# Optimization experiments

Measured on AMD Instinct MI355X. Metric: run time of the kernel, lower is better.

## Reference

```python
import jax, jax.numpy as jnp
import numpy as np

N_NODES = 8192
N_EDGES = 262144
N_REL = 8
NUM_CLASSES = 151
EMB = 256
BOX = 1024
HID = 512
OUT = 256
N_TASKS = 2


def setup_inputs() -> dict:
    key = jax.random.key(0)
    ks = jax.random.split(key, 20)
    w = lambda k, shape: jax.random.normal(k, shape, dtype=jnp.float32) * 0.02
    return {
        "box_features": jax.random.normal(ks[0], (N_NODES, BOX), dtype=jnp.float32),
        "pred_labels": jax.random.randint(ks[1], (N_NODES,), 0, NUM_CLASSES),
        "edge_index": jax.random.randint(ks[2], (2, N_EDGES), 0, N_NODES),
        "edge_type": jax.random.randint(ks[3], (N_EDGES,), 0, N_REL),
        "nodes_per_graph": 128,
        "emb_table": w(ks[4], (NUM_CLASSES, EMB)),
        "W_lin": w(ks[5], (BOX + EMB, HID)),
        "b_lin": jnp.zeros((HID,), jnp.float32),
        "rel_W1": w(ks[6], (N_REL, HID, HID)),
        "root_W1": w(ks[7], (HID, HID)),
        "b1": jnp.zeros((HID,), jnp.float32),
        "rel_W2": w(ks[8], (N_REL, HID, OUT)),
        "root_W2": w(ks[9], (HID, OUT)),
        "b2": jnp.zeros((OUT,), jnp.float32),
        "Wc1": w(ks[10], (OUT, OUT)),
        "bc1": jnp.zeros((OUT,), jnp.float32),
        "Wc2": w(ks[11], (OUT, N_TASKS)),
        "bc2": jnp.zeros((N_TASKS,), jnp.float32),
    }


def rgcn_conv(x, src, dst, etype, rel_W, root_W, b):
    """PyG RGCNConv: per-relation mean aggregation + root weight + bias."""
    R, _, out_dim = rel_W.shape
    N = x.shape[0]
    transformed = jnp.einsum('ni,rio->rno', x, rel_W)      # [R, N, out]
    msg = transformed[etype, src]                           # [E, out] gather per edge
    seg = etype * N + dst                                   # (relation, dst) segment id
    sums = jax.ops.segment_sum(msg, seg, num_segments=R * N)
    cnt = jax.ops.segment_sum(jnp.ones((msg.shape[0],), x.dtype), seg, num_segments=R * N)
    mean = sums / jnp.maximum(cnt, 1.0)[:, None]
    agg = mean.reshape(R, N, out_dim).sum(0)                # sum over relations
    return agg + x @ root_W + b


def reference(box_features, pred_labels, edge_index, edge_type, nodes_per_graph,
              emb_table, W_lin, b_lin, rel_W1, root_W1, b1, rel_W2, root_W2, b2,
              Wc1, bc1, Wc2, bc2):
    src, dst = edge_index[0], edge_index[1]
    # obj embedding + concat with box features
    x = jnp.concatenate([box_features, emb_table[pred_labels]], axis=-1)  # [N, 1280]
    x = x @ W_lin + b_lin                                                  # [N, 512]
    x = jax.nn.relu(rgcn_conv(x, src, dst, edge_type, rel_W1, root_W1, b1))
    x = rgcn_conv(x, src, dst, edge_type, rel_W2, root_W2, b2)             # [N, 256]
    # mean graph pooling over equal-size graphs
    B = x.shape[0] // nodes_per_graph
    pooled = x.reshape(B, nodes_per_graph, -1).mean(axis=1)                # [B, 256]
    # classifier (dropout is identity in eval)
    y_logits = (pooled @ Wc1 + bc1) @ Wc2 + bc2                            # [B, n_tasks]
    y_prob = jax.nn.softmax(y_logits, axis=-1)
    return y_logits, y_prob
```

## Files before the change

### kernel.cpp

```cpp
#include <hip/hip_runtime.h>
#include <cstdint>

#define NNODES 8192
#define NEDGES 262144
#define NRELS  8
#define EMBD   256
#define BOXD   1024
#define HIDD   512
#define OUTD   256
#define NSEG   (NRELS * NNODES)
#define K0DIM  (BOXD + EMBD)
#define KSDIM  (NRELS * HIDD + HIDD)

#define PREP_X0_END   8192
#define PREP_TR_END   (8192 + 2944)
#define PREP_WB_END   (8192 + 2944 + 18)
#define PREP_TOTAL    (8192 + 2944 + 18 + 1024)

using bf16x8 = __attribute__((ext_vector_type(8))) short;
using f32x4  = __attribute__((ext_vector_type(4))) float;
using us4    = __attribute__((ext_vector_type(4))) unsigned short;

__device__ __forceinline__ unsigned short f2b(float f) {
    union { float f; uint32_t u; } v; v.f = f;
    uint32_t r = v.u + 0x7FFFu + ((v.u >> 16) & 1u);
    return (unsigned short)(r >> 16);
}

__device__ __forceinline__ us4 cvt4(f32x4 v) {
    us4 u;
    u[0] = f2b(v[0]); u[1] = f2b(v[1]); u[2] = f2b(v[2]); u[3] = f2b(v[3]);
    return u;
}

__device__ __forceinline__ float b2f_lo(uint32_t w) {
    union { uint32_t u; float f; } v; v.u = w << 16; return v.f;
}
__device__ __forceinline__ float b2f_hi(uint32_t w) {
    union { uint32_t u; float f; } v; v.u = w & 0xffff0000u; return v.f;
}

__global__ __launch_bounds__(256) void k_prep(
        const float* __restrict__ box, const int* __restrict__ labels,
        const float* __restrict__ emb,
        const float* __restrict__ W_lin, const float* __restrict__ rel_W1,
        const float* __restrict__ root_W1, const float* __restrict__ rel_W2,
        const float* __restrict__ root_W2,
        const float* __restrict__ Wc1, const float* __restrict__ bc1,
        const float* __restrict__ Wc2, const float* __restrict__ bc2,
        const float* __restrict__ b2,
        const int* __restrict__ etype, const int* __restrict__ edst,
        unsigned short* __restrict__ X0, unsigned short* __restrict__ W0t,
        unsigned short* __restrict__ W1t, float* __restrict__ Wbig,
        float* __restrict__ bbig, int* __restrict__ cnt) {
    int bid = blockIdx.x;
    if (bid < PREP_X0_END) {
        int n = bid;
        int lab = labels[n];
        const f32x4* b = (const f32x4*)(box + (size_t)n * BOXD);
        const f32x4* e = (const f32x4*)(emb + (size_t)lab * EMBD);
        us4* o = (us4*)(X0 + (size_t)n * K0DIM);
        for (int j = threadIdx.x; j < K0DIM / 4; j += 256) {
            f32x4 v = (j < BOXD / 4) ? b[j] : e[j - BOXD / 4];
            o[j] = cvt4(v);
        }
    } else if (bid < PREP_TR_END) {
        __shared__ float t[32][33];
        int lb = bid - PREP_X0_END;
        const float* src; unsigned short* dst; int No, ld, kOff, kb, ob;
        if (lb < 640)       { int g = lb;        src = W_lin;   dst = W0t; No = 512; ld = K0DIM; kOff = 0;    kb = g % 40;  ob = g / 40; }
        else if (lb < 2688) { int g = lb - 640;  src = rel_W1;  dst = W1t; No = 512; ld = KSDIM; kOff = 0;    kb = g % 128; ob = g / 128; }
        else                { int g = lb - 2688; src = root_W1; dst = W1t; No = 512; ld = KSDIM; kOff = 4096; kb = g % 16;  ob = g / 16; }
        int kt = kb * 32, ot = ob * 32;
        int tx = threadIdx.x & 31, ty = threadIdx.x >> 5;
#pragma unroll
        for (int i = 0; i < 4; i++) {
            int k = kt + ty + i * 8;
            t[ty + i * 8][tx] = src[(size_t)k * No + ot + tx];
        }
        __syncthreads();
#pragma unroll
        for (int i = 0; i < 4; i++) {
            int o = ot + ty + i * 8;
            dst[(size_t)o * ld + kOff + kt + tx] = f2b(t[tx][ty + i * 8]);
        }
    } else if (bid < PREP_WB_END) {
        __shared__ float ws0[256], ws1[256];
        __shared__ float r0[256], r1[256];
        int g = bid - PREP_TR_END;
        int i = threadIdx.x;
        float w0 = 0.f, w1 = 0.f;
        for (int o = 0; o < 256; o++) {
            float c = Wc1[i * 256 + o];
            w0 += c * Wc2[o * 2 + 0];
            w1 += c * Wc2[o * 2 + 1];
        }
        ws0[i] = w0; ws1[i] = w1;
        __syncthreads();
        int k = g * 256 + i;
        const float* row = (k < 4096) ? rel_W2 + (size_t)k * 256
                                      : root_W2 + (size_t)(k - 4096) * 256;
        float s0 = 0.f, s1 = 0.f;
        for (int o = 0; o < 256; o++) {
            float v = row[o];
            s0 += v * ws0[o];
            s1 += v * ws1[o];
        }
        Wbig[k * 2 + 0] = s0;
        Wbig[k * 2 + 1] = s1;
        if (g == 0) {
            r0[i] = b2[i] * ws0[i] + bc1[i] * Wc2[i * 2 + 0];
            r1[i] = b2[i] * ws1[i] + bc1[i] * Wc2[i * 2 + 1];
            __syncthreads();
            for (int s = 128; s > 0; s >>= 1) {
                if (i < s) { r0[i] += r0[i + s]; r1[i] += r1[i + s]; }
                __syncthreads();
            }
            if (i == 0) { bbig[0] = r0[0] + bc2[0]; bbig[1] = r1[0] + bc2[1]; }
        }
    } else {
        int e = (bid - PREP_WB_END) * 256 + threadIdx.x;
        atomicAdd(&cnt[etype[e] * NNODES + edst[e]], 1);
    }
}

__global__ __launch_bounds__(1024) void k_scan(const int* __restrict__ cnt,
                                               int* __restrict__ segstart) {
    __shared__ int part[1024];
    __shared__ int sup[16];
    __shared__ int supx[16];
    int t = threadIdx.x;
    int base = t * 64;
    int s = 0;
    for (int i = 0; i < 64; i++) s += cnt[base + i];
    part[t] = s;
    __syncthreads();
    if (t < 16) {
        int a = 0;
        for (int i = 0; i < 64; i++) a += part[t * 64 + i];
        sup[t] = a;
    }
    __syncthreads();
    if (t == 0) {
        int a = 0;
        for (int i = 0; i < 16; i++) { supx[i] = a; a += sup[i]; }
    }
    __syncthreads();
    int a = supx[t >> 6];
    for (int i = (t & ~63); i < t; i++) a += part[i];
    for (int i = 0; i < 64; i++) { segstart[base + i] = a; a += cnt[base + i]; }
    if (t == 1023) segstart[NSEG] = a;
}

__global__ void k_scatter(const int* __restrict__ etype, const int* __restrict__ esrc,
                          const int* __restrict__ edst, const int* __restrict__ segstart,
                          int* __restrict__ cursor, int* __restrict__ esorted) {
    int e = blockIdx.x * 256 + threadIdx.x;
    if (e >= NEDGES) return;
    int key = etype[e] * NNODES + edst[e];
    int pos = atomicAdd(&cursor[key], 1);
    esorted[segstart[key] + pos] = esrc[e];
}

__global__ __launch_bounds__(256) void k_aggregate(
        const unsigned short* __restrict__ x, const int* __restrict__ segstart,
        const int* __restrict__ esorted, unsigned short* __restrict__ Xin) {
    int seg = blockIdx.x * 4 + (threadIdx.x >> 6);
    int lane = threadIdx.x & 63;
    int r = seg >> 13;
    int dstn = seg & (NNODES - 1);
    float a[8] = {0, 0, 0, 0, 0, 0, 0, 0};
    float b[8] = {0, 0, 0, 0, 0, 0, 0, 0};
    int s0 = segstart[seg], s1 = segstart[seg + 1];
    int t = s0;
    for (; t + 2 <= s1; t += 2) {
        uint4 v0 = *(const uint4*)(x + (size_t)esorted[t] * HIDD + lane * 8);
        uint4 v1 = *(const uint4*)(x + (size_t)esorted[t + 1] * HIDD + lane * 8);
        a[0] += b2f_lo(v0.x); a[1] += b2f_hi(v0.x);
        a[2] += b2f_lo(v0.y); a[3] += b2f_hi(v0.y);
        a[4] += b2f_lo(v0.z); a[5] += b2f_hi(v0.z);
        a[6] += b2f_lo(v0.w); a[7] += b2f_hi(v0.w);
        b[0] += b2f_lo(v1.x); b[1] += b2f_hi(v1.x);
        b[2] += b2f_lo(v1.y); b[3] += b2f_hi(v1.y);
        b[4] += b2f_lo(v1.z); b[5] += b2f_hi(v1.z);
        b[6] += b2f_lo(v1.w); b[7] += b2f_hi(v1.w);
    }
    if (t < s1) {
        uint4 v0 = *(const uint4*)(x + (size_t)esorted[t] * HIDD + lane * 8);
        a[0] += b2f_lo(v0.x); a[1] += b2f_hi(v0.x);
        a[2] += b2f_lo(v0.y); a[3] += b2f_hi(v0.y);
        a[4] += b2f_lo(v0.z); a[5] += b2f_hi(v0.z);
        a[6] += b2f_lo(v0.w); a[7] += b2f_hi(v0.w);
    }
    float iv = (s1 > s0) ? (1.0f / (float)(s1 - s0)) : 1.0f;
#pragma unroll
    for (int j = 0; j < 8; j++) a[j] = (a[j] + b[j]) * iv;
    uint4 u;
    u.x = (uint32_t)f2b(a[0]) | ((uint32_t)f2b(a[1]) << 16);
    u.y = (uint32_t)f2b(a[2]) | ((uint32_t)f2b(a[3]) << 16);
    u.z = (uint32_t)f2b(a[4]) | ((uint32_t)f2b(a[5]) << 16);
    u.w = (uint32_t)f2b(a[6]) | ((uint32_t)f2b(a[7]) << 16);
    *(uint4*)(Xin + (size_t)dstn * KSDIM + r * HIDD + lane * 8) = u;
}

__global__ __launch_bounds__(256) void k_aggpool(
        const unsigned short* __restrict__ x, const int* __restrict__ segstart,
        const int* __restrict__ esorted, float* __restrict__ PXp) {
    __shared__ float red[4][512];
    int b = blockIdx.x;
    int wave = threadIdx.x >> 6, lane = threadIdx.x & 63;
    if (b < 2048) {
        int q = b & 3, r = (b >> 2) & 7, g = b >> 5;
        float a[8] = {0, 0, 0, 0, 0, 0, 0, 0};
        int segbase = r * NNODES + g * 128 + q * 32 + wave * 8;
#pragma unroll 1
        for (int i = 0; i < 8; ++i) {
            int s0 = segstart[segbase + i], s1 = segstart[segbase + i + 1];
            if (s0 == s1) continue;
            float p[8] = {0, 0, 0, 0, 0, 0, 0, 0};
            for (int t = s0; t < s1; ++t) {
                uint4 v = *(const uint4*)(x + (size_t)esorted[t] * HIDD + lane * 8);
                p[0] += b2f_lo(v.x); p[1] += b2f_hi(v.x);
                p[2] += b2f_lo(v.y); p[3] += b2f_hi(v.y);
                p[4] += b2f_lo(v.z); p[5] += b2f_hi(v.z);
                p[6] += b2f_lo(v.w); p[7] += b2f_hi(v.w);
            }
            float w = 1.0f / (128.0f * (float)(s1 - s0));
#pragma unroll
            for (int j = 0; j < 8; j++) a[j] += p[j] * w;
        }
#pragma unroll
        for (int j = 0; j < 8; j++) red[wave][lane * 8 + j] = a[j];
        __syncthreads();
        for (int c = threadIdx.x; c < 512; c += 256) {
            float s = red[0][c] + red[1][c] + red[2][c] + red[3][c];
            PXp[((size_t)q * 64 + g) * KSDIM + r * 512 + c] = s;
        }
    } else {
        int t2 = b - 2048;
        int g = t2 >> 2, q = t2 & 3;
        float a[8] = {0, 0, 0, 0, 0, 0, 0, 0};
        int n0 = g * 128 + q * 32 + wave * 8;
#pragma unroll
        for (int i = 0; i < 8; ++i) {
            uint4 v = *(const uint4*)(x + (size_t)(n0 + i) * HIDD + lane * 8);
            a[0] += b2f_lo(v.x); a[1] += b2f_hi(v.x);
            a[2] += b2f_lo(v.y); a[3] += b2f_hi(v.y);
            a[4] += b2f_lo(v.z); a[5] += b2f_hi(v.z);
            a[6] += b2f_lo(v.w); a[7] += b2f_hi(v.w);
        }
#pragma unroll
        for (int j = 0; j < 8; j++) red[wave][lane * 8 + j] = a[j];
        __syncthreads();
        for (int c = threadIdx.x; c < 512; c += 256) {
            float s = red[0][c] + red[1][c] + red[2][c] + red[3][c];
            PXp[((size_t)q * 64 + g) * KSDIM + 4096 + c] = s * (1.0f / 128.0f);
        }
    }
}

__global__ __launch_bounds__(512, 4) void k_gemm(
        const unsigned short* __restrict__ A,
        const unsigned short* __restrict__ Bt,
        float* __restrict__ P,
        int M, int N, int K, int Kc) {
    __shared__ unsigned short As[2][128 * 64];
    __shared__ unsigned short Bs[2][128 * 64];
    const int tid = threadIdx.x;
    const int lane = tid & 63, wid = tid >> 6;
    const int tiles_m = M >> 7;
    const int tm = blockIdx.x % tiles_m, tn = blockIdx.x / tiles_m;
    const int m0 = tm << 7, n0 = tn << 7;
    const int wr = wid >> 2, wc = wid & 3;
    const int k0 = blockIdx.y * Kc;

    f32x4 acc[4][2];
#pragma unroll
    for (int i = 0; i < 4; i++)
#pragma unroll
        for (int j = 0; j < 2; j++) acc[i][j] = (f32x4){0.f, 0.f, 0.f, 0.f};

    const int rowg = tid >> 3;
    const int srcc = (tid & 7) ^ (rowg & 7);
    const unsigned short* gA = A  + (size_t)(m0 + rowg) * K + k0 + srcc * 8;
    const unsigned short* gB = Bt + (size_t)(n0 + rowg) * K + k0 + srcc * 8;
    const int ldsbase = wid * 512;

    auto stage = [&](int bsel, int kt) {
#pragma unroll
        for (int i = 0; i < 2; ++i) {
            __builtin_amdgcn_global_load_lds(
                (const __attribute__((address_space(1))) void*)(gA + kt + i * 64 * K),
                (__attribute__((address_space(3))) void*)&As[bsel][i * 4096 + ldsbase], 16, 0, 0);
            __builtin_amdgcn_global_load_lds(
                (const __attribute__((address_space(1))) void*)(gB + kt + i * 64 * K),
                (__attribute__((address_space(3))) void*)&Bs[bsel][i * 4096 + ldsbase], 16, 0, 0);
        }
    };

    const int arow = wr * 64 + (lane & 15);
    const int brow = wc * 32 + (lane & 15);
    const int l7 = lane & 7;
    const int c0 = lane >> 4;

    const int nt = Kc >> 6;
    int cur = 0;
    stage(0, 0);
    asm volatile("s_waitcnt vmcnt(0)" ::: "memory");
    __builtin_amdgcn_s_barrier();

    for (int t = 0; t < nt; ++t) {
        if (t + 1 < nt) stage(cur ^ 1, (t + 1) * 64);
#pragma unroll
        for (int s4 = 0; s4 < 2; ++s4) {
            const int slot = (c0 + s4 * 4) ^ l7;
            bf16x8 af[4], bfr[2];
#pragma unroll
            for (int m = 0; m < 4; m++)
                af[m] = *(const bf16x8*)&As[cur][(arow + m * 16) * 64 + slot * 8];
#pragma unroll
            for (int n = 0; n < 2; n++)
                bfr[n] = *(const bf16x8*)&Bs[cur][(brow + n * 16) * 64 + slot * 8];
#pragma unroll
            for (int m = 0; m < 4; m++)
#pragma unroll
                for (int n = 0; n < 2; n++)
                    acc[m][n] = __builtin_amdgcn_mfma_f32_16x16x32_bf16(af[m], bfr[n], acc[m][n], 0, 0, 0);
        }
        if (t + 1 < nt) {
            asm volatile("s_waitcnt vmcnt(0)" ::: "memory");
            __builtin_amdgcn_s_barrier();
            cur ^= 1;
        }
    }

    float* Pout = P + (size_t)blockIdx.y * M * N;
    const int crow0 = m0 + wr * 64 + (lane >> 4) * 4;
    const int ccol0 = n0 + wc * 32 + (lane & 15);
#pragma unroll
    for (int n = 0; n < 2; n++) {
        int col = ccol0 + n * 16;
#pragma unroll
        for (int m = 0; m < 4; m++)
#pragma unroll
            for (int r = 0; r < 4; r++)
                Pout[(size_t)(crow0 + m * 16 + r) * N + col] = acc[m][n][r];
    }
}

template <int RELU, int WROOT>
__global__ void k_reduce_bf(const float* __restrict__ P, const float* __restrict__ bias,
                            unsigned short* __restrict__ xbf, unsigned short* __restrict__ Xin,
                            int MN) {
    int idx = (blockIdx.x * 256 + threadIdx.x) * 4;
    f32x4 v = *(const f32x4*)&P[idx];
    v += *(const f32x4*)&P[(size_t)MN + idx];
    v += *(const f32x4*)&bias[idx & 511];
    if (RELU) {
#pragma unroll
        for (int j = 0; j < 4; j++) v[j] = fmaxf(v[j], 0.f);
    }
    us4 u = cvt4(v);
    *(us4*)&xbf[idx] = u;
    if (WROOT) {
        int row = idx >> 9, col = idx & 511;
        *(us4*)&Xin[(size_t)row * KSDIM + NRELS * HIDD + col] = u;
    }
}

__global__ void k_logits(const float* __restrict__ PXp, const float* __restrict__ Wbig,
                         const float* __restrict__ bbig, float* __restrict__ out) {
    __shared__ float r0[256], r1[256];
    int g = blockIdx.x, tid = threadIdx.x;
    const float* p0 = PXp + ((size_t)0 * 64 + g) * KSDIM;
    const float* p1 = PXp + ((size_t)1 * 64 + g) * KSDIM;
    const float* p2 = PXp + ((size_t)2 * 64 + g) * KSDIM;
    const float* p3 = PXp + ((size_t)3 * 64 + g) * KSDIM;
    float s0 = 0.f, s1 = 0.f;
#pragma unroll
    for (int i = 0; i < 18; i++) {
        int k = i * 256 + tid;
        float px = p0[k] + p1[k] + p2[k] + p3[k];
        s0 += px * Wbig[k * 2 + 0];
        s1 += px * Wbig[k * 2 + 1];
    }
    r0[tid] = s0; r1[tid] = s1;
    __syncthreads();
    for (int s = 128; s > 0; s >>= 1) {
        if (tid < s) { r0[tid] += r0[tid + s]; r1[tid] += r1[tid + s]; }
        __syncthreads();
    }
    if (tid == 0) {
        float l0 = r0[0] + bbig[0], l1 = r1[0] + bbig[1];
        out[g * 2 + 0] = l0;
        out[g * 2 + 1] = l1;
        float m = fmaxf(l0, l1);
        float e0 = expf(l0 - m), e1 = expf(l1 - m);
        float inv = 1.0f / (e0 + e1);
        out[128 + g * 2 + 0] = e0 * inv;
        out[128 + g * 2 + 1] = e1 * inv;
    }
}

extern "C" void kernel_launch(void* const* d_in, const int* in_sizes, int n_in,
                              void* d_out, int out_size, void* d_ws, size_t ws_size,
                              hipStream_t stream) {
    const float* box     = (const float*)d_in[0];
    const int*   labels  = (const int*)d_in[1];
    const int*   eidx    = (const int*)d_in[2];
    const int*   etype   = (const int*)d_in[3];
    const float* emb     = (const float*)d_in[5];
    const float* W_lin   = (const float*)d_in[6];
    const float* b_lin   = (const float*)d_in[7];
    const float* rel_W1  = (const float*)d_in[8];
    const float* root_W1 = (const float*)d_in[9];
    const float* b1      = (const float*)d_in[10];
    const float* rel_W2  = (const float*)d_in[11];
    const float* root_W2 = (const float*)d_in[12];
    const float* b2      = (const float*)d_in[13];
    const float* Wc1     = (const float*)d_in[14];
    const float* bc1     = (const float*)d_in[15];
    const float* Wc2     = (const float*)d_in[16];
    const float* bc2     = (const float*)d_in[17];
    const int* esrc = eidx;
    const int* edst = eidx + NEDGES;

    char* ws = (char*)d_ws;
    size_t off = 0;
    auto alloc = [&](size_t bytes) -> char* {
        char* p = ws + off;
        off += (bytes + 255) & ~(size_t)255;
        return p;
    };
    float* Pp = (float*)alloc((size_t)2 * NNODES * HIDD * 4);
    unsigned short* Xin = (unsigned short*)alloc((size_t)NNODES * KSDIM * 2);
    unsigned short* X0  = Xin;
    unsigned short* xbf = (unsigned short*)alloc((size_t)NNODES * HIDD * 2);
    unsigned short* W0t = (unsigned short*)alloc((size_t)HIDD * K0DIM * 2);
    unsigned short* W1t = (unsigned short*)alloc((size_t)HIDD * KSDIM * 2);
    float* PXp    = (float*)alloc((size_t)4 * 64 * KSDIM * 4);
    float* Wbig   = (float*)alloc((size_t)KSDIM * 2 * 4);
    float* bbig   = (float*)alloc(2 * 4);
    int*   cnt     = (int*)alloc((size_t)NSEG * 4);
    int*   cursor  = (int*)alloc((size_t)NSEG * 4);
    int*   segst   = (int*)alloc((size_t)(NSEG + 1) * 4);
    int*   esorted = (int*)alloc((size_t)NEDGES * 4);
    if (off > ws_size) return;

    float* out = (float*)d_out;
    const int MN = NNODES * HIDD;

    hipMemsetAsync(cnt, 0, (size_t)2 * NSEG * 4, stream);
    k_prep<<<PREP_TOTAL, 256, 0, stream>>>(
        box, labels, emb, W_lin, rel_W1, root_W1, rel_W2, root_W2,
        Wc1, bc1, Wc2, bc2, b2, etype, edst,
        X0, W0t, W1t, Wbig, bbig, cnt);
    k_scan<<<1, 1024, 0, stream>>>(cnt, segst);
    k_scatter<<<NEDGES / 256, 256, 0, stream>>>(etype, esrc, edst, segst, cursor, esorted);

    k_gemm<<<dim3((NNODES / 128) * (HIDD / 128), 2), 512, 0, stream>>>(
        X0, W0t, Pp, NNODES, HIDD, K0DIM, K0DIM / 2);
    k_reduce_bf<0, 1><<<MN / 1024, 256, 0, stream>>>(Pp, b_lin, xbf, Xin, MN);

    k_aggregate<<<NSEG / 4, 256, 0, stream>>>(xbf, segst, esorted, Xin);
    k_gemm<<<dim3((NNODES / 128) * (HIDD / 128), 2), 512, 0, stream>>>(
        Xin, W1t, Pp, NNODES, HIDD, KSDIM, KSDIM / 2);
    k_reduce_bf<1, 0><<<MN / 1024, 256, 0, stream>>>(Pp, b1, xbf, Xin, MN);

    k_aggpool<<<2048 + 256, 256, 0, stream>>>(xbf, segst, esorted, PXp);
    k_logits<<<64, 256, 0, stream>>>(PXp, Wbig, bbig, out);
}
```

Before: 258.7 us.

## Replace second-layer gather-pool with dense coefficient-matrix GEMM

The final aggregate-and-pool step is recast as a dense matrix product. A per-(relation, graph) by source-node coefficient matrix is built during the edge scatter with atomics, converted to bf16, and multiplied by a transposed hidden-feature matrix using the existing split-K GEMM. The root term is folded into the logits kernel. This removes the irregular per-edge gathers in pooling, but adds a 16MB memset, atomic scatter traffic, a conversion pass, a transpose, and bf16 rounding of the coefficients.

```diff
diff --git a/kernel.cpp b/kernel.cpp
--- a/kernel.cpp
+++ b/kernel.cpp
@@ -16,6 +16,8 @@
 #define PREP_TR_END   (8192 + 2944)
 #define PREP_WB_END   (8192 + 2944 + 18)
 #define PREP_TOTAL    (8192 + 2944 + 18 + 1024)
+
+#define PX_SPLITS 16
 
 using bf16x8 = __attribute__((ext_vector_type(8))) short;
 using f32x4  = __attribute__((ext_vector_type(4))) float;
@@ -154,12 +156,23 @@
 
 __global__ void k_scatter(const int* __restrict__ etype, const int* __restrict__ esrc,
                           const int* __restrict__ edst, const int* __restrict__ segstart,
-                          int* __restrict__ cursor, int* __restrict__ esorted) {
+                          int* __restrict__ cursor, int* __restrict__ esorted,
+                          float* __restrict__ Cf) {
     int e = blockIdx.x * 256 + threadIdx.x;
     if (e >= NEDGES) return;
-    int key = etype[e] * NNODES + edst[e];
+    int r = etype[e], d = edst[e], s = esrc[e];
+    int key = r * NNODES + d;
     int pos = atomicAdd(&cursor[key], 1);
-    esorted[segstart[key] + pos] = esrc[e];
+    esorted[segstart[key] + pos] = s;
+    int cntv = segstart[key + 1] - segstart[key];
+    float w = 1.0f / (128.0f * (float)cntv);
+    atomicAdd(&Cf[(size_t)(r * 64 + (d >> 7)) * NNODES + s], w);
+}
+
+__global__ void k_c2bf(const float* __restrict__ Cf, unsigned short* __restrict__ Cbf) {
+    int idx = (blockIdx.x * 256 + threadIdx.x) * 4;
+    f32x4 v = *(const f32x4*)&Cf[idx];
+    *(us4*)&Cbf[idx] = cvt4(v);
 }
 
 __global__ __launch_bounds__(256) void k_aggregate(
@@ -203,60 +216,18 @@
     *(uint4*)(Xin + (size_t)dstn * KSDIM + r * HIDD + lane * 8) = u;
 }
 
-__global__ __launch_bounds__(256) void k_aggpool(
-        const unsigned short* __restrict__ x, const int* __restrict__ segstart,
-        const int* __restrict__ esorted, float* __restrict__ PXp) {
-    __shared__ float red[4][512];
+__global__ void k_xT(const unsigned short* __restrict__ xbf, unsigned short* __restrict__ xT) {
+    __shared__ unsigned short t[32][33];
     int b = blockIdx.x;
-    int wave = threadIdx.x >> 6, lane = threadIdx.x & 63;
-    if (b < 2048) {
-        int q = b & 3, r = (b >> 2) & 7, g = b >> 5;
-        float a[8] = {0, 0, 0, 0, 0, 0, 0, 0};
-        int segbase = r * NNODES + g * 128 + q * 32 + wave * 8;
-#pragma unroll 1
-        for (int i = 0; i < 8; ++i) {
-            int s0 = segstart[segbase + i], s1 = segstart[segbase + i + 1];
-            if (s0 == s1) continue;
-            float p[8] = {0, 0, 0, 0, 0, 0, 0, 0};
-            for (int t = s0; t < s1; ++t) {
-                uint4 v = *(const uint4*)(x + (size_t)esorted[t] * HIDD + lane * 8);
-                p[0] += b2f_lo(v.x); p[1] += b2f_hi(v.x);
-                p[2] += b2f_lo(v.y); p[3] += b2f_hi(v.y);
-                p[4] += b2f_lo(v.z); p[5] += b2f_hi(v.z);
-                p[6] += b2f_lo(v.w); p[7] += b2f_hi(v.w);
-            }
-            float w = 1.0f / (128.0f * (float)(s1 - s0));
-#pragma unroll
-            for (int j = 0; j < 8; j++) a[j] += p[j] * w;
-        }
-#pragma unroll
-        for (int j = 0; j < 8; j++) red[wave][lane * 8 + j] = a[j];
-        __syncthreads();
-        for (int c = threadIdx.x; c < 512; c += 256) {
-            float s = red[0][c] + red[1][c] + red[2][c] + red[3][c];
-            PXp[((size_t)q * 64 + g) * KSDIM + r * 512 + c] = s;
-        }
-    } else {
-        int t2 = b - 2048;
-        int g = t2 >> 2, q = t2 & 3;
-        float a[8] = {0, 0, 0, 0, 0, 0, 0, 0};
-        int n0 = g * 128 + q * 32 + wave * 8;
-#pragma unroll
-        for (int i = 0; i < 8; ++i) {
-            uint4 v = *(const uint4*)(x + (size_t)(n0 + i) * HIDD + lane * 8);
-            a[0] += b2f_lo(v.x); a[1] += b2f_hi(v.x);
-            a[2] += b2f_lo(v.y); a[3] += b2f_hi(v.y);
-            a[4] += b2f_lo(v.z); a[5] += b2f_hi(v.z);
-            a[6] += b2f_lo(v.w); a[7] += b2f_hi(v.w);
-        }
-#pragma unroll
-        for (int j = 0; j < 8; j++) red[wave][lane * 8 + j] = a[j];
-        __syncthreads();
-        for (int c = threadIdx.x; c < 512; c += 256) {
-            float s = red[0][c] + red[1][c] + red[2][c] + red[3][c];
-            PXp[((size_t)q * 64 + g) * KSDIM + 4096 + c] = s * (1.0f / 128.0f);
-        }
-    }
+    int rt = (b & 255) * 32, ct = (b >> 8) * 32;
+    int tx = threadIdx.x & 31, ty = threadIdx.x >> 5;
+#pragma unroll
+    for (int i = 0; i < 4; i++)
+        t[ty + i * 8][tx] = xbf[(size_t)(rt + ty + i * 8) * HIDD + ct + tx];
+    __syncthreads();
+#pragma unroll
+    for (int i = 0; i < 4; i++)
+        xT[(size_t)(ct + ty + i * 8) * NNODES + rt + tx] = t[tx][ty + i * 8];
 }
 
 __global__ __launch_bounds__(512, 4) void k_gemm(
@@ -368,22 +339,48 @@
     }
 }
 
-__global__ void k_logits(const float* __restrict__ PXp, const float* __restrict__ Wbig,
-                         const float* __restrict__ bbig, float* __restrict__ out) {
+__global__ __launch_bounds__(256) void k_logits(
+        const float* __restrict__ P, const unsigned short* __restrict__ xbf,
+        const float* __restrict__ Wbig, const float* __restrict__ bbig,
+        float* __restrict__ out) {
     __shared__ float r0[256], r1[256];
+    __shared__ float wr0[512], wr1[512];
     int g = blockIdx.x, tid = threadIdx.x;
-    const float* p0 = PXp + ((size_t)0 * 64 + g) * KSDIM;
-    const float* p1 = PXp + ((size_t)1 * 64 + g) * KSDIM;
-    const float* p2 = PXp + ((size_t)2 * 64 + g) * KSDIM;
-    const float* p3 = PXp + ((size_t)3 * 64 + g) * KSDIM;
+    for (int c = tid; c < 512; c += 256) {
+        wr0[c] = Wbig[(4096 + c) * 2 + 0];
+        wr1[c] = Wbig[(4096 + c) * 2 + 1];
+    }
     float s0 = 0.f, s1 = 0.f;
 #pragma unroll
-    for (int i = 0; i < 18; i++) {
-        int k = i * 256 + tid;
-        float px = p0[k] + p1[k] + p2[k] + p3[k];
-        s0 += px * Wbig[k * 2 + 0];
-        s1 += px * Wbig[k * 2 + 1];
-    }
+    for (int r = 0; r < 8; r++) {
+        const float* pr = P + (size_t)(r * 64 + g) * 512;
+        for (int c = tid; c < 512; c += 256) {
+            float px = 0.f;
+#pragma unroll
+            for (int s = 0; s < PX_SPLITS; s++) px += pr[(size_t)s * 512 * 512 + c];
+            s0 += px * Wbig[(r * 512 + c) * 2 + 0];
+            s1 += px * Wbig[(r * 512 + c) * 2 + 1];
+        }
+    }
+    __syncthreads();
+    int n = g * 128 + (tid >> 1);
+    int cbase = (tid & 1) * 256;
+    const unsigned short* xr = xbf + (size_t)n * HIDD + cbase;
+    float t0 = 0.f, t1 = 0.f;
+    for (int c = 0; c < 256; c += 8) {
+        uint4 v = *(const uint4*)(xr + c);
+        float x0 = b2f_lo(v.x), x1 = b2f_hi(v.x);
+        float x2 = b2f_lo(v.y), x3 = b2f_hi(v.y);
+        float x4 = b2f_lo(v.z), x5 = b2f_hi(v.z);
+        float x6 = b2f_lo(v.w), x7 = b2f_hi(v.w);
+        int cc = cbase + c;
+        t0 += x0 * wr0[cc] + x1 * wr0[cc + 1] + x2 * wr0[cc + 2] + x3 * wr0[cc + 3]
+            + x4 * wr0[cc + 4] + x5 * wr0[cc + 5] + x6 * wr0[cc + 6] + x7 * wr0[cc + 7];
+        t1 += x0 * wr1[cc] + x1 * wr1[cc + 1] + x2 * wr1[cc + 2] + x3 * wr1[cc + 3]
+            + x4 * wr1[cc + 4] + x5 * wr1[cc + 5] + x6 * wr1[cc + 6] + x7 * wr1[cc + 7];
+    }
+    s0 += t0 * (1.0f / 128.0f);
+    s1 += t1 * (1.0f / 128.0f);
     r0[tid] = s0; r1[tid] = s1;
     __syncthreads();
     for (int s = 128; s > 0; s >>= 1) {
@@ -433,12 +430,14 @@
         return p;
     };
     float* Pp = (float*)alloc((size_t)2 * NNODES * HIDD * 4);
+    float* Cf = Pp;
     unsigned short* Xin = (unsigned short*)alloc((size_t)NNODES * KSDIM * 2);
     unsigned short* X0  = Xin;
+    unsigned short* xT  = (unsigned short*)Xin;
     unsigned short* xbf = (unsigned short*)alloc((size_t)NNODES * HIDD * 2);
     unsigned short* W0t = (unsigned short*)alloc((size_t)HIDD * K0DIM * 2);
     unsigned short* W1t = (unsigned short*)alloc((size_t)HIDD * KSDIM * 2);
-    float* PXp    = (float*)alloc((size_t)4 * 64 * KSDIM * 4);
+    unsigned short* Cbf = (unsigned short*)alloc((size_t)512 * NNODES * 2);
     float* Wbig   = (float*)alloc((size_t)KSDIM * 2 * 4);
     float* bbig   = (float*)alloc(2 * 4);
     int*   cnt     = (int*)alloc((size_t)NSEG * 4);
@@ -451,12 +450,14 @@
     const int MN = NNODES * HIDD;
 
     hipMemsetAsync(cnt, 0, (size_t)2 * NSEG * 4, stream);
+    hipMemsetAsync(Cf, 0, (size_t)512 * NNODES * 4, stream);
     k_prep<<<PREP_TOTAL, 256, 0, stream>>>(
         box, labels, emb, W_lin, rel_W1, root_W1, rel_W2, root_W2,
         Wc1, bc1, Wc2, bc2, b2, etype, edst,
         X0, W0t, W1t, Wbig, bbig, cnt);
     k_scan<<<1, 1024, 0, stream>>>(cnt, segst);
-    k_scatter<<<NEDGES / 256, 256, 0, stream>>>(etype, esrc, edst, segst, cursor, esorted);
+    k_scatter<<<NEDGES / 256, 256, 0, stream>>>(etype, esrc, edst, segst, cursor, esorted, Cf);
+    k_c2bf<<<512 * NNODES / 1024, 256, 0, stream>>>(Cf, Cbf);
 
     k_gemm<<<dim3((NNODES / 128) * (HIDD / 128), 2), 512, 0, stream>>>(
         X0, W0t, Pp, NNODES, HIDD, K0DIM, K0DIM / 2);
@@ -467,6 +468,8 @@
         Xin, W1t, Pp, NNODES, HIDD, KSDIM, KSDIM / 2);
     k_reduce_bf<1, 0><<<MN / 1024, 256, 0, stream>>>(Pp, b1, xbf, Xin, MN);
 
-    k_aggpool<<<2048 + 256, 256, 0, stream>>>(xbf, segst, esorted, PXp);
-    k_logits<<<64, 256, 0, stream>>>(PXp, Wbig, bbig, out);
-}
+    k_xT<<<4096, 256, 0, stream>>>(xbf, xT);
+    k_gemm<<<dim3((512 / 128) * (512 / 128), PX_SPLITS), 512, 0, stream>>>(
+        Cbf, xT, Pp, 512, 512, NNODES, NNODES / PX_SPLITS);
+    k_logits<<<64, 256, 0, stream>>>(Pp, xbf, Wbig, bbig, out);
+}
```

Measured after the change: 272.6 us (median of 2 runs). 1.05x slower.

## Enlarge GEMM tile to 256x128 with triple-buffered LDS pipeline and split pooling kernel

Applied to the files above, without the earlier changes.

The GEMM tile grows from 128x128 to 256x128, so each of the 8 waves computes a 64x64 sub-tile with 16 accumulators. The LDS pipeline moves from double to triple buffering with partial vmcnt waits and s_setprio around the MFMA block, to hide load latency and raise operand reuse. In exchange LDS use rises to 144 KB, occupancy drops to 2 blocks per CU, and the grid halves, which may leave CUs idle. The aggregate-pool kernel is also split into separate aggregation and root-pool kernels, which adds one more launch.

```diff
diff --git a/kernel.cpp b/kernel.cpp
--- a/kernel.cpp
+++ b/kernel.cpp
@@ -206,79 +206,81 @@
 __global__ __launch_bounds__(256) void k_aggpool(
         const unsigned short* __restrict__ x, const int* __restrict__ segstart,
         const int* __restrict__ esorted, float* __restrict__ PXp) {
+    int b = blockIdx.x;
+    int q = b & 3, r = (b >> 2) & 7, g = b >> 5;
+    int wave = threadIdx.x >> 6, lane = threadIdx.x & 63;
+    float a[8] = {0, 0, 0, 0, 0, 0, 0, 0};
+    int segbase = r * NNODES + g * 128 + q * 32 + wave * 8;
+#pragma unroll 1
+    for (int i = 0; i < 8; ++i) {
+        int s0 = segstart[segbase + i], s1 = segstart[segbase + i + 1];
+        if (s0 == s1) continue;
+        float p[8] = {0, 0, 0, 0, 0, 0, 0, 0};
+        for (int t = s0; t < s1; ++t) {
+            uint4 v = *(const uint4*)(x + (size_t)esorted[t] * HIDD + lane * 8);
+            p[0] += b2f_lo(v.x); p[1] += b2f_hi(v.x);
+            p[2] += b2f_lo(v.y); p[3] += b2f_hi(v.y);
+            p[4] += b2f_lo(v.z); p[5] += b2f_hi(v.z);
+            p[6] += b2f_lo(v.w); p[7] += b2f_hi(v.w);
+        }
+        float w = 1.0f / (128.0f * (float)(s1 - s0));
+#pragma unroll
+        for (int j = 0; j < 8; j++) a[j] += p[j] * w;
+    }
     __shared__ float red[4][512];
-    int b = blockIdx.x;
+#pragma unroll
+    for (int j = 0; j < 8; j++) red[wave][lane * 8 + j] = a[j];
+    __syncthreads();
+    for (int c = threadIdx.x; c < 512; c += 256) {
+        float s = red[0][c] + red[1][c] + red[2][c] + red[3][c];
+        PXp[((size_t)q * 64 + g) * KSDIM + r * 512 + c] = s;
+    }
+}
+
+__global__ __launch_bounds__(256) void k_rootpool(
+        const unsigned short* __restrict__ x, float* __restrict__ PXp) {
+    int g = blockIdx.x >> 2, q = blockIdx.x & 3;
     int wave = threadIdx.x >> 6, lane = threadIdx.x & 63;
-    if (b < 2048) {
-        int q = b & 3, r = (b >> 2) & 7, g = b >> 5;
-        float a[8] = {0, 0, 0, 0, 0, 0, 0, 0};
-        int segbase = r * NNODES + g * 128 + q * 32 + wave * 8;
-#pragma unroll 1
-        for (int i = 0; i < 8; ++i) {
-            int s0 = segstart[segbase + i], s1 = segstart[segbase + i + 1];
-            if (s0 == s1) continue;
-            float p[8] = {0, 0, 0, 0, 0, 0, 0, 0};
-            for (int t = s0; t < s1; ++t) {
-                uint4 v = *(const uint4*)(x + (size_t)esorted[t] * HIDD + lane * 8);
-                p[0] += b2f_lo(v.x); p[1] += b2f_hi(v.x);
-                p[2] += b2f_lo(v.y); p[3] += b2f_hi(v.y);
-                p[4] += b2f_lo(v.z); p[5] += b2f_hi(v.z);
-                p[6] += b2f_lo(v.w); p[7] += b2f_hi(v.w);
-            }
-            float w = 1.0f / (128.0f * (float)(s1 - s0));
-#pragma unroll
-            for (int j = 0; j < 8; j++) a[j] += p[j] * w;
-        }
-#pragma unroll
-        for (int j = 0; j < 8; j++) red[wave][lane * 8 + j] = a[j];
-        __syncthreads();
-        for (int c = threadIdx.x; c < 512; c += 256) {
-            float s = red[0][c] + red[1][c] + red[2][c] + red[3][c];
-            PXp[((size_t)q * 64 + g) * KSDIM + r * 512 + c] = s;
-        }
-    } else {
-        int t2 = b - 2048;
-        int g = t2 >> 2, q = t2 & 3;
-        float a[8] = {0, 0, 0, 0, 0, 0, 0, 0};
-        int n0 = g * 128 + q * 32 + wave * 8;
-#pragma unroll
-        for (int i = 0; i < 8; ++i) {
-            uint4 v = *(const uint4*)(x + (size_t)(n0 + i) * HIDD + lane * 8);
-            a[0] += b2f_lo(v.x); a[1] += b2f_hi(v.x);
-            a[2] += b2f_lo(v.y); a[3] += b2f_hi(v.y);
-            a[4] += b2f_lo(v.z); a[5] += b2f_hi(v.z);
-            a[6] += b2f_lo(v.w); a[7] += b2f_hi(v.w);
-        }
-#pragma unroll
-        for (int j = 0; j < 8; j++) red[wave][lane * 8 + j] = a[j];
-        __syncthreads();
-        for (int c = threadIdx.x; c < 512; c += 256) {
-            float s = red[0][c] + red[1][c] + red[2][c] + red[3][c];
-            PXp[((size_t)q * 64 + g) * KSDIM + 4096 + c] = s * (1.0f / 128.0f);
-        }
-    }
-}
-
-__global__ __launch_bounds__(512, 4) void k_gemm(
+    float a[8] = {0, 0, 0, 0, 0, 0, 0, 0};
+    int n0 = g * 128 + q * 32 + wave * 8;
+#pragma unroll
+    for (int i = 0; i < 8; ++i) {
+        uint4 v = *(const uint4*)(x + (size_t)(n0 + i) * HIDD + lane * 8);
+        a[0] += b2f_lo(v.x); a[1] += b2f_hi(v.x);
+        a[2] += b2f_lo(v.y); a[3] += b2f_hi(v.y);
+        a[4] += b2f_lo(v.z); a[5] += b2f_hi(v.z);
+        a[6] += b2f_lo(v.w); a[7] += b2f_hi(v.w);
+    }
+    __shared__ float red[4][512];
+#pragma unroll
+    for (int j = 0; j < 8; j++) red[wave][lane * 8 + j] = a[j];
+    __syncthreads();
+    for (int c = threadIdx.x; c < 512; c += 256) {
+        float s = red[0][c] + red[1][c] + red[2][c] + red[3][c];
+        PXp[((size_t)q * 64 + g) * KSDIM + 4096 + c] = s * (1.0f / 128.0f);
+    }
+}
+
+__global__ __launch_bounds__(512, 2) void k_gemm(
         const unsigned short* __restrict__ A,
         const unsigned short* __restrict__ Bt,
         float* __restrict__ P,
         int M, int N, int K, int Kc) {
-    __shared__ unsigned short As[2][128 * 64];
-    __shared__ unsigned short Bs[2][128 * 64];
+    __shared__ unsigned short As[3][256 * 64];
+    __shared__ unsigned short Bs[3][128 * 64];
     const int tid = threadIdx.x;
     const int lane = tid & 63, wid = tid >> 6;
-    const int tiles_m = M >> 7;
+    const int tiles_m = M >> 8;
     const int tm = blockIdx.x % tiles_m, tn = blockIdx.x / tiles_m;
-    const int m0 = tm << 7, n0 = tn << 7;
-    const int wr = wid >> 2, wc = wid & 3;
+    const int m0 = tm << 8, n0 = tn << 7;
+    const int wr = wid >> 1, wc = wid & 1;
     const int k0 = blockIdx.y * Kc;
 
-    f32x4 acc[4][2];
+    f32x4 acc[4][4];
 #pragma unroll
     for (int i = 0; i < 4; i++)
 #pragma unroll
-        for (int j = 0; j < 2; j++) acc[i][j] = (f32x4){0.f, 0.f, 0.f, 0.f};
+        for (int j = 0; j < 4; j++) acc[i][j] = (f32x4){0.f, 0.f, 0.f, 0.f};
 
     const int rowg = tid >> 3;
     const int srcc = (tid & 7) ^ (rowg & 7);
@@ -288,57 +290,67 @@
 
     auto stage = [&](int bsel, int kt) {
 #pragma unroll
-        for (int i = 0; i < 2; ++i) {
+        for (int i = 0; i < 4; ++i)
             __builtin_amdgcn_global_load_lds(
-                (const __attribute__((address_space(1))) void*)(gA + kt + i * 64 * K),
+                (const __attribute__((address_space(1))) void*)(gA + kt + (size_t)i * 64 * K),
                 (__attribute__((address_space(3))) void*)&As[bsel][i * 4096 + ldsbase], 16, 0, 0);
+#pragma unroll
+        for (int i = 0; i < 2; ++i)
             __builtin_amdgcn_global_load_lds(
-                (const __attribute__((address_space(1))) void*)(gB + kt + i * 64 * K),
+                (const __attribute__((address_space(1))) void*)(gB + kt + (size_t)i * 64 * K),
                 (__attribute__((address_space(3))) void*)&Bs[bsel][i * 4096 + ldsbase], 16, 0, 0);
-        }
     };
 
     const int arow = wr * 64 + (lane & 15);
-    const int brow = wc * 32 + (lane & 15);
+    const int brow = wc * 64 + (lane & 15);
     const int l7 = lane & 7;
     const int c0 = lane >> 4;
 
     const int nt = Kc >> 6;
-    int cur = 0;
     stage(0, 0);
-    asm volatile("s_waitcnt vmcnt(0)" ::: "memory");
+    if (nt > 1) {
+        stage(1, 64);
+        asm volatile("s_waitcnt vmcnt(6)" ::: "memory");
+    } else {
+        asm volatile("s_waitcnt vmcnt(0)" ::: "memory");
+    }
     __builtin_amdgcn_s_barrier();
 
     for (int t = 0; t < nt; ++t) {
-        if (t + 1 < nt) stage(cur ^ 1, (t + 1) * 64);
+        const int cur = t % 3;
+        if (t + 2 < nt) stage((t + 2) % 3, (t + 2) * 64);
+        __builtin_amdgcn_s_setprio(1);
 #pragma unroll
         for (int s4 = 0; s4 < 2; ++s4) {
             const int slot = (c0 + s4 * 4) ^ l7;
-            bf16x8 af[4], bfr[2];
+            bf16x8 af[4], bfr[4];
 #pragma unroll
             for (int m = 0; m < 4; m++)
                 af[m] = *(const bf16x8*)&As[cur][(arow + m * 16) * 64 + slot * 8];
 #pragma unroll
-            for (int n = 0; n < 2; n++)
+            for (int n = 0; n < 4; n++)
                 bfr[n] = *(const bf16x8*)&Bs[cur][(brow + n * 16) * 64 + slot * 8];
 #pragma unroll
             for (int m = 0; m < 4; m++)
 #pragma unroll
-                for (int n = 0; n < 2; n++)
+                for (int n = 0; n < 4; n++)
                     acc[m][n] = __builtin_amdgcn_mfma_f32_16x16x32_bf16(af[m], bfr[n], acc[m][n], 0, 0, 0);
         }
+        __builtin_amdgcn_s_setprio(0);
         if (t + 1 < nt) {
-            asm volatile("s_waitcnt vmcnt(0)" ::: "memory");
+            if (t + 2 < nt)
+                asm volatile("s_waitcnt vmcnt(6)" ::: "memory");
+            else
+                asm volatile("s_waitcnt vmcnt(0)" ::: "memory");
             __builtin_amdgcn_s_barrier();
-            cur ^= 1;
         }
     }
 
     float* Pout = P + (size_t)blockIdx.y * M * N;
     const int crow0 = m0 + wr * 64 + (lane >> 4) * 4;
-    const int ccol0 = n0 + wc * 32 + (lane & 15);
-#pragma unroll
-    for (int n = 0; n < 2; n++) {
+    const int ccol0 = n0 + wc * 64 + (lane & 15);
+#pragma unroll
+    for (int n = 0; n < 4; n++) {
         int col = ccol0 + n * 16;
 #pragma unroll
         for (int m = 0; m < 4; m++)
@@ -458,15 +470,16 @@
     k_scan<<<1, 1024, 0, stream>>>(cnt, segst);
     k_scatter<<<NEDGES / 256, 256, 0, stream>>>(etype, esrc, edst, segst, cursor, esorted);
 
-    k_gemm<<<dim3((NNODES / 128) * (HIDD / 128), 2), 512, 0, stream>>>(
+    k_gemm<<<dim3((NNODES / 256) * (HIDD / 128), 2), 512, 0, stream>>>(
         X0, W0t, Pp, NNODES, HIDD, K0DIM, K0DIM / 2);
     k_reduce_bf<0, 1><<<MN / 1024, 256, 0, stream>>>(Pp, b_lin, xbf, Xin, MN);
 
     k_aggregate<<<NSEG / 4, 256, 0, stream>>>(xbf, segst, esorted, Xin);
-    k_gemm<<<dim3((NNODES / 128) * (HIDD / 128), 2), 512, 0, stream>>>(
+    k_gemm<<<dim3((NNODES / 256) * (HIDD / 128), 2), 512, 0, stream>>>(
         Xin, W1t, Pp, NNODES, HIDD, KSDIM, KSDIM / 2);
     k_reduce_bf<1, 0><<<MN / 1024, 256, 0, stream>>>(Pp, b1, xbf, Xin, MN);
 
-    k_aggpool<<<2048 + 256, 256, 0, stream>>>(xbf, segst, esorted, PXp);
+    k_aggpool<<<2048, 256, 0, stream>>>(xbf, segst, esorted, PXp);
+    k_rootpool<<<256, 256, 0, stream>>>(xbf, PXp);
     k_logits<<<64, 256, 0, stream>>>(PXp, Wbig, bbig, out);
 }
```

After: 257.3 us. No clear change (-0.5%).
